# Kernel tuning notes

Hardware: AMD Instinct MI355X
Metric: run time of the kernel (lower is better)

Reference implementation:

```python
import jax, jax.numpy as jnp
import numpy as np

DIM = 1024
HEADS = 16
HEAD_DIM = DIM // HEADS
K = 13              # kernel_size (odd)
NS = K // 2         # neighborhood radius
SCALE = HEAD_DIM ** -0.5


def setup_inputs() -> dict:
    key = jax.random.key(0)
    ks = jax.random.split(key, 5)
    B, L = 2, 4096
    x = jax.random.normal(ks[0], (B, L, DIM), jnp.float32)
    qkv_w = jax.random.normal(ks[1], (3 * DIM, DIM), jnp.float32) * 0.02
    qkv_b = jnp.zeros((3 * DIM,), jnp.float32)
    rpb = jax.random.normal(ks[2], (HEADS, 2 * K - 1), jnp.float32) * 0.02  # trunc_normal std=0.02
    proj_w = jax.random.normal(ks[3], (DIM, DIM), jnp.float32) * 0.02
    proj_b = jnp.zeros((DIM,), jnp.float32)
    return dict(x=x, qkv_w=qkv_w, qkv_b=qkv_b, rpb=rpb, proj_w=proj_w, proj_b=proj_b)


def reference(x, qkv_w, qkv_b, rpb, proj_w, proj_b):
    B, L, C = x.shape
    # qkv projection (torch Linear convention: y = x @ W^T + b)
    qkv = (x @ qkv_w.T + qkv_b).reshape(B, L, 3, HEADS, HEAD_DIM).transpose(2, 0, 3, 1, 4)
    q, k, v = qkv[0] * SCALE, qkv[1], qkv[2]  # each [B, H, L, D]

    i = jnp.arange(L)
    # NATTEN 1D window start (dilation=1): clamp window fully inside [0, L)
    ni = jnp.clip(i - NS, 0, L - K)                       # [L]
    # relative-position-bias start index per query (NATTEN get_pb_start)
    pi = NS + jnp.where(i < NS, NS - i, 0) + jnp.where(i + NS >= L, L - i - 1 - NS, 0)  # [L]
    j = jnp.arange(K)
    nbr = ni[:, None] + j[None, :]                        # [L, K] neighbor key indices
    bidx = pi[:, None] + j[None, :]                       # [L, K] rpb indices in [0, 2K-2]

    kg = k[:, :, nbr, :]                                  # [B, H, L, K, D]
    vg = v[:, :, nbr, :]                                  # [B, H, L, K, D]

    attn = jnp.einsum('bhld,bhlkd->bhlk', q, kg) + rpb[:, bidx][None]  # [B, H, L, K]
    attn = jax.nn.softmax(attn, axis=-1)
    out = jnp.einsum('bhlk,bhlkd->bhld', attn, vg)        # [B, H, L, D]
    out = out.transpose(0, 2, 1, 3).reshape(B, L, C)
    return out @ proj_w.T + proj_b
```

## Files before the change

### kernel.cpp

```cpp
#include <hip/hip_runtime.h>
#include <hip/hip_bf16.h>

#define DIMC 1024
#define HEADS 16
#define HEAD_DIM 64
#define KWIN 13
#define NSH 6
#define LSEQ 4096
#define BATCH 2
#define NROWS (BATCH*LSEQ)
#define QKV_N (3*DIMC)
#define SCALE_Q 0.125f

#define TBLK 256
#define WROWS 268

typedef __attribute__((ext_vector_type(4))) float f32x4;
typedef __attribute__((ext_vector_type(8))) short bf16x8;

__device__ __forceinline__ void gload_lds16(const void* g, void* l) {
  __builtin_amdgcn_global_load_lds(
      (const __attribute__((address_space(1))) void*)g,
      (__attribute__((address_space(3))) void*)l, 16, 0, 0);
}

__device__ __forceinline__ void cvt8(uint4 r, float* f) {
  unsigned u[4] = {r.x, r.y, r.z, r.w};
#pragma unroll
  for (int w = 0; w < 4; w++) {
    f[2*w]   = __uint_as_float(u[w] << 16);
    f[2*w+1] = __uint_as_float(u[w] & 0xffff0000u);
  }
}

__global__ __launch_bounds__(256) void cast3_kernel(const float* __restrict__ in0, __hip_bfloat16* __restrict__ out0, int n0,
                                                    const float* __restrict__ in1, __hip_bfloat16* __restrict__ out1, int n1,
                                                    const float* __restrict__ in2, __hip_bfloat16* __restrict__ out2, int n2) {
  int i = blockIdx.x * 256 + threadIdx.x;
  const float* in; __hip_bfloat16* out; int k;
  if (i < n0) { in = in0; out = out0; k = i; }
  else if (i < n0 + n1) { in = in1; out = out1; k = i - n0; }
  else if (i < n0 + n1 + n2) { in = in2; out = out2; k = i - n0 - n1; }
  else return;
  float4 v = ((const float4*)in)[k];
  union { short4 s; __hip_bfloat16 h[4]; } u;
  u.h[0] = __float2bfloat16(v.x);
  u.h[1] = __float2bfloat16(v.y);
  u.h[2] = __float2bfloat16(v.z);
  u.h[3] = __float2bfloat16(v.w);
  ((short4*)out)[k] = u.s;
}


#define STAGE4(s) do { \
  __hip_bfloat16* dst_ = smem + (s) * 8192 + wave * 1024; \
  gload_lds16(gA,       dst_); \
  gload_lds16(gA + r16, dst_ + 512); \
  gload_lds16(gB,       dst_ + 4096); \
  gload_lds16(gB + r16, dst_ + 4096 + 512); \
} while (0)

#define COMPUTE16(s) do { \
  const __hip_bfloat16* As_ = smem + (s) * 8192; \
  const __hip_bfloat16* Bs_ = As_ + 4096; \
  bf16x8 af[4], bfr[4]; \
  _Pragma("unroll") for (int i = 0; i < 4; i++) \
    af[i] = *(const bf16x8*)&As_[(wr * 64 + i * 16 + fr) * 32 + fk0]; \
  _Pragma("unroll") for (int i = 0; i < 4; i++) \
    bfr[i] = *(const bf16x8*)&Bs_[(wc * 64 + i * 16 + fr) * 32 + fk0]; \
  _Pragma("unroll") for (int mi = 0; mi < 4; mi++) \
  _Pragma("unroll") for (int ni = 0; ni < 4; ni++) \
    acc[mi][ni] = __builtin_amdgcn_mfma_f32_16x16x32_bf16(af[mi], bfr[ni], acc[mi][ni], 0, 0, 0); \
} while (0)

template<int OUT_BF16>
__global__ __launch_bounds__(256) void gemm_bt(const __hip_bfloat16* __restrict__ A,
                                               const __hip_bfloat16* __restrict__ B,
                                               const float* __restrict__ bias,
                                               void* __restrict__ Cout,
                                               int M, int N, int K) {
  __shared__ __align__(16) __hip_bfloat16 smem[16384];

  const int tid  = threadIdx.x;
  const int lane = tid & 63;
  const int wave = tid >> 6;
  const int m0 = blockIdx.y * 128;
  const int n0 = blockIdx.x * 128;
  const int wr = wave >> 1;
  const int wc = wave & 1;

  f32x4 acc[4][4] = {};

  const int rA0  = wave * 32 + (lane >> 2);
  const int kcol = ((lane & 3) ^ ((lane >> 3) & 3)) * 8;
  const __hip_bfloat16* gA = A + (size_t)(m0 + rA0) * K + kcol;
  const __hip_bfloat16* gB = B + (size_t)(n0 + rA0) * K + kcol;
  const size_t r16 = (size_t)16 * K;

  const int fr  = lane & 15;
  const int fq  = lane >> 4;
  const int fk0 = ((fq ^ ((fr >> 1) & 3)) & 3) * 8;

  const int NT = K >> 5;

  STAGE4(0);
  gA += 32; gB += 32;
  __syncthreads();

  int cur = 0;
#pragma unroll 1
  for (int t = 1; t < NT; t++) {
    STAGE4(cur ^ 1);
    gA += 32; gB += 32;
    COMPUTE16(cur);
    __syncthreads();
    cur ^= 1;
  }
  COMPUTE16(cur);

#pragma unroll
  for (int ni = 0; ni < 4; ni++) {
    const int col = n0 + wc * 64 + ni * 16 + (lane & 15);
    const float bv = bias[col];
#pragma unroll
    for (int mi = 0; mi < 4; mi++) {
      const int row = m0 + wr * 64 + mi * 16 + ((lane >> 4) << 2);
#pragma unroll
      for (int i = 0; i < 4; i++) {
        const float v = acc[mi][ni][i] + bv;
        if (OUT_BF16)
          ((__hip_bfloat16*)Cout)[(size_t)(row + i) * N + col] = __float2bfloat16(v);
        else
          ((float*)Cout)[(size_t)(row + i) * N + col] = v;
      }
    }
  }
}

__global__ __launch_bounds__(256, 2) void natten(const __hip_bfloat16* __restrict__ qkv,
                                                 const float* __restrict__ rpb,
                                                 __hip_bfloat16* __restrict__ att) {
  __shared__ __align__(16) unsigned char smem[2 * WROWS * 128];

  const int tid = threadIdx.x;
  const int tb  = blockIdx.x;
  const int h   = blockIdx.y;
  const int b   = blockIdx.z;
  const int t0  = tb * TBLK;

  int r0 = t0 - NSH;
  if (r0 < 0) r0 = 0;
  if (r0 > LSEQ - WROWS) r0 = LSEQ - WROWS;

  const __hip_bfloat16* kg = qkv + ((size_t)b * LSEQ + r0) * QKV_N + DIMC + h * HEAD_DIM;
  const __hip_bfloat16* vg = kg + DIMC;
#pragma unroll 1
  for (int i = tid; i < WROWS * 8; i += 256) {
    const int row = i >> 3, c = i & 7;
    const uint4 kk = *(const uint4*)(kg + (size_t)row * QKV_N + c * 8);
    const uint4 vv = *(const uint4*)(vg + (size_t)row * QKV_N + c * 8);
    const int off = row * 128 + ((c * 16) ^ ((row & 7) << 4));
    *(uint4*)(smem + off) = kk;
    *(uint4*)(smem + WROWS * 128 + off) = vv;
  }
  __syncthreads();

  const int t = t0 + tid;
  int ni = t - NSH;
  ni = ni < 0 ? 0 : (ni > LSEQ - KWIN ? LSEQ - KWIN : ni);
  const int rbase = ni - r0;
  const int pi = NSH + (t < NSH ? NSH - t : 0) + (t + NSH >= LSEQ ? LSEQ - t - 1 - NSH : 0);
  const float* rp = rpb + h * (2 * KWIN - 1) + pi;

  const __hip_bfloat16* qg = qkv + ((size_t)b * LSEQ + t) * QKV_N + h * HEAD_DIM;
  float qf[64];
#pragma unroll
  for (int c = 0; c < 8; c++) {
    uint4 qq = *(const uint4*)(qg + c * 8);
    cvt8(qq, qf + c * 8);
  }

  float p[KWIN];
#pragma unroll
  for (int j = 0; j < KWIN; j++) {
    const int row = rbase + j;
    const int sw = (row & 7) << 4;
    float s = 0.f;
#pragma unroll
    for (int c = 0; c < 8; c++) {
      uint4 kk = *(const uint4*)(smem + row * 128 + ((c * 16) ^ sw));
      float kf[8];
      cvt8(kk, kf);
#pragma unroll
      for (int e = 0; e < 8; e++) s += qf[c * 8 + e] * kf[e];
    }
    p[j] = s * SCALE_Q + rp[j];
  }

  float m = p[0];
#pragma unroll
  for (int j = 1; j < KWIN; j++) m = fmaxf(m, p[j]);
  float sum = 0.f;
#pragma unroll
  for (int j = 0; j < KWIN; j++) { p[j] = __expf(p[j] - m); sum += p[j]; }
  const float inv = 1.f / sum;
#pragma unroll
  for (int j = 0; j < KWIN; j++) p[j] *= inv;

  __hip_bfloat16* og = att + ((size_t)b * LSEQ + t) * DIMC + h * HEAD_DIM;
#pragma unroll
  for (int c = 0; c < 8; c++) {
    float acc[8] = {0.f, 0.f, 0.f, 0.f, 0.f, 0.f, 0.f, 0.f};
#pragma unroll
    for (int j = 0; j < KWIN; j++) {
      const int row = rbase + j;
      uint4 vv = *(const uint4*)(smem + WROWS * 128 + row * 128 + ((c * 16) ^ ((row & 7) << 4)));
      float vf[8];
      cvt8(vv, vf);
#pragma unroll
      for (int e = 0; e < 8; e++) acc[e] += p[j] * vf[e];
    }
    union { ushort us[8]; uint4 v; } o;
#pragma unroll
    for (int e = 0; e < 8; e++) {
      __hip_bfloat16 hb = __float2bfloat16(acc[e]);
      o.us[e] = *(ushort*)&hb;
    }
    *(uint4*)(og + c * 8) = o.v;
  }
}

extern "C" void kernel_launch(void* const* d_in, const int* in_sizes, int n_in,
                              void* d_out, int out_size, void* d_ws, size_t ws_size,
                              hipStream_t stream) {
  const float* x      = (const float*)d_in[0];
  const float* qkv_w  = (const float*)d_in[1];
  const float* qkv_b  = (const float*)d_in[2];
  const float* rpb    = (const float*)d_in[3];
  const float* proj_w = (const float*)d_in[4];
  const float* proj_b = (const float*)d_in[5];
  float* out = (float*)d_out;

  char* ws = (char*)d_ws;
  __hip_bfloat16* xb    = (__hip_bfloat16*)(ws);
  __hip_bfloat16* wqkv  = (__hip_bfloat16*)(ws + 16777216);
  __hip_bfloat16* wproj = (__hip_bfloat16*)(ws + 23068672);
  __hip_bfloat16* qkv   = (__hip_bfloat16*)(ws + 25165824);
  __hip_bfloat16* att   = (__hip_bfloat16*)(ws + 75497472);

  const int n0 = NROWS * DIMC / 4;
  const int n1 = QKV_N * DIMC / 4;
  const int n2 = DIMC * DIMC / 4;
  cast3_kernel<<<(n0 + n1 + n2 + 255) / 256, 256, 0, stream>>>(
      x, xb, n0, qkv_w, wqkv, n1, proj_w, wproj, n2);

  gemm_bt<1><<<dim3(QKV_N / 128, NROWS / 128), 256, 0, stream>>>(
      xb, wqkv, qkv_b, (void*)qkv, NROWS, QKV_N, DIMC);

  natten<<<dim3(LSEQ / TBLK, HEADS, BATCH), 256, 0, stream>>>(qkv, rpb, att);

  gemm_bt<0><<<dim3(DIMC / 128, NROWS / 128), 256, 0, stream>>>(
      att, wproj, proj_b, (void*)out, NROWS, DIMC, DIMC);
}
```

Before: 137.5 us.

## Remap GEMM workgroups per XCD and widen cast to 8 elements per thread

The GEMM launches become 1D grids, and block ids are remapped so each XCD processes a contiguous range of output tiles. This is meant to improve L2 reuse of the A and B operands across neighbouring tiles. The fp32-to-bf16 cast kernel now converts 8 elements per thread with 16-byte stores, which halves the thread count. The remap changes tile traversal order, which could instead increase cache conflicts depending on the resulting tile pattern.

```diff
diff --git a/kernel.cpp b/kernel.cpp
--- a/kernel.cpp
+++ b/kernel.cpp
@@ -42,13 +42,19 @@
   else if (i < n0 + n1) { in = in1; out = out1; k = i - n0; }
   else if (i < n0 + n1 + n2) { in = in2; out = out2; k = i - n0 - n1; }
   else return;
-  float4 v = ((const float4*)in)[k];
-  union { short4 s; __hip_bfloat16 h[4]; } u;
-  u.h[0] = __float2bfloat16(v.x);
-  u.h[1] = __float2bfloat16(v.y);
-  u.h[2] = __float2bfloat16(v.z);
-  u.h[3] = __float2bfloat16(v.w);
-  ((short4*)out)[k] = u.s;
+  const float4* p = (const float4*)in + (size_t)k * 2;
+  float4 a = p[0], b = p[1];
+  union { ushort us[8]; uint4 v; } o;
+  __hip_bfloat16 h;
+  h = __float2bfloat16(a.x); o.us[0] = *(ushort*)&h;
+  h = __float2bfloat16(a.y); o.us[1] = *(ushort*)&h;
+  h = __float2bfloat16(a.z); o.us[2] = *(ushort*)&h;
+  h = __float2bfloat16(a.w); o.us[3] = *(ushort*)&h;
+  h = __float2bfloat16(b.x); o.us[4] = *(ushort*)&h;
+  h = __float2bfloat16(b.y); o.us[5] = *(ushort*)&h;
+  h = __float2bfloat16(b.z); o.us[6] = *(ushort*)&h;
+  h = __float2bfloat16(b.w); o.us[7] = *(ushort*)&h;
+  ((uint4*)out)[k] = o.v;
 }
 
 
@@ -78,14 +84,24 @@
                                                const __hip_bfloat16* __restrict__ B,
                                                const float* __restrict__ bias,
                                                void* __restrict__ Cout,
-                                               int M, int N, int K) {
+                                               int M, int N, int K, int nbx) {
   __shared__ __align__(16) __hip_bfloat16 smem[16384];
 
   const int tid  = threadIdx.x;
   const int lane = tid & 63;
   const int wave = tid >> 6;
-  const int m0 = blockIdx.y * 128;
-  const int n0 = blockIdx.x * 128;
+
+  int id = blockIdx.x;
+  {
+    const int nwg = gridDim.x;
+    const int q = nwg >> 3, r = nwg & 7;
+    const int xcd = id & 7, off = id >> 3;
+    id = (xcd < r ? xcd * (q + 1) : r * (q + 1) + (xcd - r) * q) + off;
+  }
+  const int bx = id % nbx;
+  const int by = id / nbx;
+  const int m0 = by * 128;
+  const int n0 = bx * 128;
   const int wr = wave >> 1;
   const int wc = wave & 1;
 
@@ -248,17 +264,17 @@
   __hip_bfloat16* qkv   = (__hip_bfloat16*)(ws + 25165824);
   __hip_bfloat16* att   = (__hip_bfloat16*)(ws + 75497472);
 
-  const int n0 = NROWS * DIMC / 4;
-  const int n1 = QKV_N * DIMC / 4;
-  const int n2 = DIMC * DIMC / 4;
+  const int n0 = NROWS * DIMC / 8;
+  const int n1 = QKV_N * DIMC / 8;
+  const int n2 = DIMC * DIMC / 8;
   cast3_kernel<<<(n0 + n1 + n2 + 255) / 256, 256, 0, stream>>>(
       x, xb, n0, qkv_w, wqkv, n1, proj_w, wproj, n2);
 
-  gemm_bt<1><<<dim3(QKV_N / 128, NROWS / 128), 256, 0, stream>>>(
-      xb, wqkv, qkv_b, (void*)qkv, NROWS, QKV_N, DIMC);
+  gemm_bt<1><<<(QKV_N / 128) * (NROWS / 128), 256, 0, stream>>>(
+      xb, wqkv, qkv_b, (void*)qkv, NROWS, QKV_N, DIMC, QKV_N / 128);
 
   natten<<<dim3(LSEQ / TBLK, HEADS, BATCH), 256, 0, stream>>>(qkv, rpb, att);
 
-  gemm_bt<0><<<dim3(DIMC / 128, NROWS / 128), 256, 0, stream>>>(
-      att, wproj, proj_b, (void*)out, NROWS, DIMC, DIMC);
-}
+  gemm_bt<0><<<(DIMC / 128) * (NROWS / 128), 256, 0, stream>>>(
+      att, wproj, proj_b, (void*)out, NROWS, DIMC, DIMC, DIMC / 128);
+}
```

New measurement: 134.5 us, median of 2. 2.1% less time.
